# Kernel tuning notes

Measured on AMD Instinct MI355X. Metric: run time of the kernel, lower is better.

## Reference

```python
import jax, jax.numpy as jnp
import numpy as np

N_NODES = 50000
N_EDGES = 1600000
IN_DIM = 128
OUT_DIM = 128
NUM_HEADS = 4
HEAD_DIM = OUT_DIM // NUM_HEADS


def setup_inputs() -> dict:
    key = jax.random.key(0)
    ks = jax.random.split(key, 10)
    s_in = 1.0 / np.sqrt(IN_DIM)
    s_out = 1.0 / np.sqrt(OUT_DIM)
    return {
        "x": jax.random.normal(ks[0], (N_NODES, IN_DIM), dtype=jnp.float32),
        "edge_index": jax.random.randint(ks[1], (2, N_EDGES), 0, N_NODES, dtype=jnp.int64),
        "Wq": jax.random.uniform(ks[2], (OUT_DIM, IN_DIM), jnp.float32, -s_in, s_in),
        "bq": jax.random.uniform(ks[3], (OUT_DIM,), jnp.float32, -s_in, s_in),
        "Wk": jax.random.uniform(ks[4], (OUT_DIM, IN_DIM), jnp.float32, -s_in, s_in),
        "bk": jax.random.uniform(ks[5], (OUT_DIM,), jnp.float32, -s_in, s_in),
        "Wv": jax.random.uniform(ks[6], (OUT_DIM, IN_DIM), jnp.float32, -s_in, s_in),
        "bv": jax.random.uniform(ks[7], (OUT_DIM,), jnp.float32, -s_in, s_in),
        "Wo": jax.random.uniform(ks[8], (OUT_DIM, OUT_DIM), jnp.float32, -s_out, s_out),
        "bo": jax.random.uniform(ks[9], (OUT_DIM,), jnp.float32, -s_out, s_out),
    }


def reference(x, edge_index, Wq, bq, Wk, bk, Wv, bv, Wo, bo):
    n = x.shape[0]
    # node-level projections -> [N, H, Hd]
    Q = (x @ Wq.T + bq).reshape(n, NUM_HEADS, HEAD_DIM)
    K = (x @ Wk.T + bk).reshape(n, NUM_HEADS, HEAD_DIM)
    V = (x @ Wv.T + bv).reshape(n, NUM_HEADS, HEAD_DIM)
    src, dst = edge_index[0], edge_index[1]
    # edge scores: [E, H]
    scores = (Q[dst] * K[src]).sum(-1) / np.sqrt(HEAD_DIM).astype(np.float32)
    # global-max shifted exp (faithful to original, which uses a single global max)
    scores_exp = jnp.exp(scores - scores.max())
    # per-dst normalization: [N, H]
    scores_sum = jax.ops.segment_sum(scores_exp, dst, num_segments=n)
    attention = scores_exp / (scores_sum[dst] + 1e-8)  # dropout in eval mode = identity
    # weighted aggregate of V[src] into dst: [N, H, Hd]
    messages = V[src] * attention[:, :, None]
    out = jax.ops.segment_sum(messages, dst, num_segments=n)
    out = out.reshape(n, OUT_DIM) @ Wo.T + bo
    return jax.nn.relu(out)
```

## Files before the change

### kernel.cpp

```cpp
#include <hip/hip_runtime.h>

#define N_NODES 50000
#define N_EDGES 1600000
#define DIM 128
#define M_PAD 50048
#define SCAN_NB ((N_NODES + 255) / 256)

#define OFF_WCATB  0UL
#define OFF_BCAT   98304UL
#define OFF_XB     99840UL
#define OFF_C      12912128UL
#define OFF_SRC    64112128UL
#define OFF_RANK   67312128UL
#define OFF_RS     70512128UL
#define OFF_CNT    70712136UL
#define OFF_BSUM   70912136UL
#define OFF_AGG    70913168UL

typedef __attribute__((ext_vector_type(8))) short short8;
typedef __attribute__((ext_vector_type(4))) float floatx4;

__device__ __forceinline__ unsigned bf16r(float f) {
    unsigned u = __float_as_uint(f);
    return (u + 0x7fffu + ((u >> 16) & 1u)) >> 16;
}
__device__ __forceinline__ unsigned pack2(float a, float b) {
    return bf16r(a) | (bf16r(b) << 16);
}
__device__ __forceinline__ float blo(unsigned v) { return __uint_as_float(v << 16); }
__device__ __forceinline__ float bhi(unsigned v) { return __uint_as_float(v & 0xffff0000u); }

#define CVT_NB 6250
#define ZERO_NB SCAN_NB
#define PREPW_NB 192
__global__ __launch_bounds__(256) void k_prep(const float* __restrict__ x,
                                              unsigned short* __restrict__ xb,
                                              int* __restrict__ counts,
                                              const float* __restrict__ Wq, const float* __restrict__ bq,
                                              const float* __restrict__ Wk, const float* __restrict__ bk,
                                              const float* __restrict__ Wv, const float* __restrict__ bv,
                                              unsigned short* __restrict__ Wcatb,
                                              float* __restrict__ bcat) {
    int bx = blockIdx.x, t = threadIdx.x;
    if (bx < CVT_NB) {
        int i = bx * 256 + t;
        if (i < N_NODES * DIM / 4) {
            float4 f = ((const float4*)x)[i];
            ushort4 o;
            o.x = (unsigned short)bf16r(f.x); o.y = (unsigned short)bf16r(f.y);
            o.z = (unsigned short)bf16r(f.z); o.w = (unsigned short)bf16r(f.w);
            ((ushort4*)xb)[i] = o;
        }
    } else if (bx < CVT_NB + ZERO_NB) {
        int i = (bx - CVT_NB) * 256 + t;
        if (i < N_NODES) counts[i] = 0;
    } else {
        int i = (bx - CVT_NB - ZERO_NB) * 256 + t;
        if (i < 3 * DIM * DIM) {
            int ro = i >> 7, col = i & 127;
            const float* W = (ro < 128) ? Wq : (ro < 256) ? Wk : Wv;
            Wcatb[i] = (unsigned short)bf16r(W[(ro & 127) * DIM + col]);
        }
        if (i < 3 * DIM) {
            const float* b = (i < 128) ? bq : (i < 256) ? bk : bv;
            bcat[i] = b[i & 127];
        }
    }
}

#define GQ_MB (M_PAD / 64)
#define GQ_BLOCKS (GQ_MB * 6)
#define HIST_NB 6250
#define GQH_GRID (1564 * 7)
__global__ __launch_bounds__(256) void k_gemmqkv_hist(const unsigned short* __restrict__ xb,
                                                      const unsigned short* __restrict__ Wb,
                                                      const float* __restrict__ bias,
                                                      unsigned* __restrict__ Cu, int M,
                                                      const int* __restrict__ dstA,
                                                      int* __restrict__ counts,
                                                      unsigned short* __restrict__ rank16) {
    __shared__ __align__(16) unsigned short As[64][136];
    __shared__ __align__(16) unsigned short Bs[64][136];
    const int grp = blockIdx.x / 7, r = blockIdx.x % 7;
    if (r >= 3) {
        int h = grp * 4 + (r - 3);
        if (h < HIST_NB) {
            int e = h * 256 + threadIdx.x;
            if (e < N_EDGES) rank16[e] = (unsigned short)atomicAdd(&counts[dstA[e]], 1);
        }
        return;
    }
    const int g = grp * 3 + r;
    const int m0 = (g % GQ_MB) * 64, n0 = (g / GQ_MB) * 64;
    const int t = threadIdx.x;
    {
        int row = t >> 2, ch = t & 3;
        const uint4* xrow = (const uint4*)(xb + (long)(m0 + row) * 128);
        const uint4* wrow = (const uint4*)(Wb + (long)(n0 + row) * 128);
#pragma unroll
        for (int j = 0; j < 4; ++j) {
            *(uint4*)&As[row][(ch + 4 * j) * 8] = xrow[ch + 4 * j];
            *(uint4*)&Bs[row][(ch + 4 * j) * 8] = wrow[ch + 4 * j];
        }
    }
    __syncthreads();
    const int w = t >> 6, lane = t & 63;
    const int quad = lane >> 4, c = lane & 15;
    floatx4 acc[4] = {{0.f,0.f,0.f,0.f},{0.f,0.f,0.f,0.f},{0.f,0.f,0.f,0.f},{0.f,0.f,0.f,0.f}};
#pragma unroll
    for (int ks = 0; ks < 4; ++ks) {
        short8 a = *(const short8*)&As[w * 16 + c][ks * 32 + quad * 8];
#pragma unroll
        for (int nt = 0; nt < 4; ++nt) {
            short8 b = *(const short8*)&Bs[nt * 16 + c][ks * 32 + quad * 8];
            acc[nt] = __builtin_amdgcn_mfma_f32_16x16x32_bf16(a, b, acc[nt], 0, 0, 0);
        }
    }
#pragma unroll
    for (int nt = 0; nt < 4; ++nt) {
        int gn = n0 + nt * 16 + c;
        float bv = bias[gn];
        int slice = gn >> 7;
        int cs = gn & 127;
#pragma unroll
        for (int i = 0; i < 4; ++i) {
            int gm = m0 + w * 16 + quad * 4 + i;
            float o = acc[nt][i] + bv;
            float f1 = __shfl_xor(o, 1);
            float f2 = __shfl_xor(o, 2);
            float f3 = __shfl_xor(o, 3);
            if (gm < M) {
                unsigned* crow = Cu + (long)gm * 256;
                if (slice == 0) {
                    ((float*)crow)[cs] = o;
                } else if (slice == 1) {
                    if ((c & 3) == 0) {
                        int pk = __builtin_amdgcn_cvt_pk_fp8_f32(o, f1, 0, false);
                        pk = __builtin_amdgcn_cvt_pk_fp8_f32(f2, f3, pk, true);
                        crow[128 + (cs >> 2)] = (unsigned)pk;
                    }
                } else {
                    if ((c & 1) == 0) crow[160 + (cs >> 1)] = pack2(o, f1);
                }
            }
        }
    }
}

__global__ __launch_bounds__(256) void k_scanA(const int* __restrict__ counts,
                                               int* __restrict__ bsum) {
    __shared__ int red[256];
    int t = threadIdx.x, i = blockIdx.x * 256 + t;
    red[t] = (i < N_NODES) ? counts[i] : 0;
    __syncthreads();
    for (int off = 128; off > 0; off >>= 1) {
        if (t < off) red[t] += red[t + off];
        __syncthreads();
    }
    if (t == 0) bsum[blockIdx.x] = red[0];
}
__global__ __launch_bounds__(256) void k_scanB(int* __restrict__ bsum, int nb) {
    __shared__ int s[256];
    int t = threadIdx.x;
    int v = (t < nb) ? bsum[t] : 0;
    s[t] = v;
    __syncthreads();
    for (int off = 1; off < 256; off <<= 1) {
        int u = (t >= off) ? s[t - off] : 0;
        __syncthreads();
        s[t] += u;
        __syncthreads();
    }
    if (t < nb) bsum[t] = s[t] - v;
}
__global__ __launch_bounds__(256) void k_scanC(const int* __restrict__ counts,
                                               const int* __restrict__ bsum,
                                               int* __restrict__ row_start) {
    __shared__ int s[256];
    int t = threadIdx.x, i = blockIdx.x * 256 + t;
    int v = (i < N_NODES) ? counts[i] : 0;
    s[t] = v;
    __syncthreads();
    for (int off = 1; off < 256; off <<= 1) {
        int u = (t >= off) ? s[t - off] : 0;
        __syncthreads();
        s[t] += u;
        __syncthreads();
    }
    int excl = bsum[blockIdx.x] + s[t] - v;
    if (i < N_NODES) {
        row_start[i] = excl;
        if (i == N_NODES - 1) row_start[N_NODES] = excl + v;
    }
}

__global__ void k_fill(const int* __restrict__ srcA, const int* __restrict__ dstA,
                       const int* __restrict__ row_start,
                       const unsigned short* __restrict__ rank16,
                       unsigned short* __restrict__ csr_src) {
    int e = blockIdx.x * blockDim.x + threadIdx.x;
    if (e < N_EDGES) {
        int d = dstA[e];
        csr_src[row_start[d] + rank16[e]] = (unsigned short)srcA[e];
    }
}

__global__ __launch_bounds__(256) void k_attn(const unsigned* __restrict__ Cu,
                                              const int* __restrict__ row_start,
                                              const unsigned short* __restrict__ csr_src,
                                              float* __restrict__ agg) {
    int d = blockIdx.x * 4 + (threadIdx.x >> 6);
    int lane = threadIdx.x & 63;
    if (d >= N_NODES) return;
    const int half = lane >> 5, sl = lane & 31;
    const float scale = 0.17677669529663687f;
    float4 q4 = *(const float4*)((const float*)(Cu + (long)d * 256) + 4 * sl);
    q4.x *= scale; q4.y *= scale; q4.z *= scale; q4.w *= scale;
    int s0 = row_start[d], s1 = row_start[d + 1];
    float lsum = 0.f, a0 = 0.f, a1 = 0.f, a2 = 0.f, a3 = 0.f;
    int pos = s0;
    for (; pos + 4 <= s1; pos += 4) {
        int sa = csr_src[pos + half];
        int sb = csr_src[pos + 2 + half];
        const unsigned* ra = Cu + (long)sa * 256;
        const unsigned* rb = Cu + (long)sb * 256;
        unsigned ka = ra[128 + sl];
        unsigned kb = rb[128 + sl];
        uint2 va = *(const uint2*)(ra + 160 + 2 * sl);
        uint2 vb = *(const uint2*)(rb + 160 + 2 * sl);
        float pa = q4.x * __builtin_amdgcn_cvt_f32_fp8(ka, 0)
                 + q4.y * __builtin_amdgcn_cvt_f32_fp8(ka, 1)
                 + q4.z * __builtin_amdgcn_cvt_f32_fp8(ka, 2)
                 + q4.w * __builtin_amdgcn_cvt_f32_fp8(ka, 3);
        float pb = q4.x * __builtin_amdgcn_cvt_f32_fp8(kb, 0)
                 + q4.y * __builtin_amdgcn_cvt_f32_fp8(kb, 1)
                 + q4.z * __builtin_amdgcn_cvt_f32_fp8(kb, 2)
                 + q4.w * __builtin_amdgcn_cvt_f32_fp8(kb, 3);
        pa += __shfl_xor(pa, 1); pa += __shfl_xor(pa, 2); pa += __shfl_xor(pa, 4);
        pb += __shfl_xor(pb, 1); pb += __shfl_xor(pb, 2); pb += __shfl_xor(pb, 4);
        float wa = __expf(pa), wb = __expf(pb);
        lsum += wa + wb;
        a0 += wa * blo(va.x) + wb * blo(vb.x);
        a1 += wa * bhi(va.x) + wb * bhi(vb.x);
        a2 += wa * blo(va.y) + wb * blo(vb.y);
        a3 += wa * bhi(va.y) + wb * bhi(vb.y);
    }
    for (; pos < s1; pos += 2) {
        int e = pos + half;
        bool ok = e < s1;
        int sa = csr_src[ok ? e : (s1 - 1)];
        const unsigned* ra = Cu + (long)sa * 256;
        unsigned ka = ra[128 + sl];
        uint2 va = *(const uint2*)(ra + 160 + 2 * sl);
        float pa = q4.x * __builtin_amdgcn_cvt_f32_fp8(ka, 0)
                 + q4.y * __builtin_amdgcn_cvt_f32_fp8(ka, 1)
                 + q4.z * __builtin_amdgcn_cvt_f32_fp8(ka, 2)
                 + q4.w * __builtin_amdgcn_cvt_f32_fp8(ka, 3);
        pa += __shfl_xor(pa, 1); pa += __shfl_xor(pa, 2); pa += __shfl_xor(pa, 4);
        float wa = ok ? __expf(pa) : 0.f;
        lsum += wa;
        a0 += wa * blo(va.x);
        a1 += wa * bhi(va.x);
        a2 += wa * blo(va.y);
        a3 += wa * bhi(va.y);
    }
    lsum += __shfl_xor(lsum, 32);
    a0 += __shfl_xor(a0, 32);
    a1 += __shfl_xor(a1, 32);
    a2 += __shfl_xor(a2, 32);
    a3 += __shfl_xor(a3, 32);
    if (lane < 32) {
        float inv = 1.f / (lsum + 1e-8f);
        float4 o;
        o.x = a0 * inv; o.y = a1 * inv; o.z = a2 * inv; o.w = a3 * inv;
        *(float4*)&agg[(long)d * 128 + 4 * sl] = o;
    }
}

__global__ __launch_bounds__(256) void k_gemm(const float* __restrict__ A,
                                              const float* __restrict__ B,
                                              const float* __restrict__ bias,
                                              float* __restrict__ Cp, int M) {
    __shared__ float As[32][64];
    __shared__ float Bs[32][64];
    const int m0 = blockIdx.x * 64, n0 = blockIdx.y * 64;
    const int t = threadIdx.x;
    const int tm = (t & 15) * 4, tn = (t >> 4) * 4;
    float acc[4][4] = {};
    for (int k0 = 0; k0 < 128; k0 += 32) {
#pragma unroll
        for (int i = 0; i < 2; ++i) {
            int idx = t + i * 256;
            int row = idx >> 3;
            int c4 = (idx & 7) * 4;
            float4 fa = make_float4(0.f, 0.f, 0.f, 0.f);
            if (m0 + row < M) fa = *(const float4*)&A[(long)(m0 + row) * 128 + k0 + c4];
            As[c4 + 0][row] = fa.x; As[c4 + 1][row] = fa.y;
            As[c4 + 2][row] = fa.z; As[c4 + 3][row] = fa.w;
            float4 fb = *(const float4*)&B[(long)(n0 + row) * 128 + k0 + c4];
            Bs[c4 + 0][row] = fb.x; Bs[c4 + 1][row] = fb.y;
            Bs[c4 + 2][row] = fb.z; Bs[c4 + 3][row] = fb.w;
        }
        __syncthreads();
#pragma unroll
        for (int k = 0; k < 32; ++k) {
            float4 a = *(const float4*)&As[k][tm];
            float4 b = *(const float4*)&Bs[k][tn];
            acc[0][0] += a.x * b.x; acc[0][1] += a.x * b.y; acc[0][2] += a.x * b.z; acc[0][3] += a.x * b.w;
            acc[1][0] += a.y * b.x; acc[1][1] += a.y * b.y; acc[1][2] += a.y * b.z; acc[1][3] += a.y * b.w;
            acc[2][0] += a.z * b.x; acc[2][1] += a.z * b.y; acc[2][2] += a.z * b.z; acc[2][3] += a.z * b.w;
            acc[3][0] += a.w * b.x; acc[3][1] += a.w * b.y; acc[3][2] += a.w * b.z; acc[3][3] += a.w * b.w;
        }
        __syncthreads();
    }
    float4 bv4 = *(const float4*)&bias[n0 + tn];
#pragma unroll
    for (int i = 0; i < 4; ++i) {
        int m = m0 + tm + i;
        if (m >= M) continue;
        float4 o;
        o.x = fmaxf(acc[i][0] + bv4.x, 0.f); o.y = fmaxf(acc[i][1] + bv4.y, 0.f);
        o.z = fmaxf(acc[i][2] + bv4.z, 0.f); o.w = fmaxf(acc[i][3] + bv4.w, 0.f);
        *(float4*)&Cp[(long)m * 128 + n0 + tn] = o;
    }
}

extern "C" void kernel_launch(void* const* d_in, const int* in_sizes, int n_in,
                              void* d_out, int out_size, void* d_ws, size_t ws_size,
                              hipStream_t stream) {
    const float* x  = (const float*)d_in[0];
    const int* edge = (const int*)d_in[1];
    const float* Wq = (const float*)d_in[2];
    const float* bq = (const float*)d_in[3];
    const float* Wk = (const float*)d_in[4];
    const float* bk = (const float*)d_in[5];
    const float* Wv = (const float*)d_in[6];
    const float* bv = (const float*)d_in[7];
    const float* Wo = (const float*)d_in[8];
    const float* bo = (const float*)d_in[9];
    float* out = (float*)d_out;

    char* ws = (char*)d_ws;
    unsigned short* Wcatb = (unsigned short*)(ws + OFF_WCATB);
    float* bcat      = (float*)(ws + OFF_BCAT);
    unsigned short* xb = (unsigned short*)(ws + OFF_XB);
    unsigned* Cu     = (unsigned*)(ws + OFF_C);
    unsigned short* csr_src = (unsigned short*)(ws + OFF_SRC);
    unsigned short* rank16  = (unsigned short*)(ws + OFF_RANK);
    int*   row_start = (int*)(ws + OFF_RS);
    int*   counts    = (int*)(ws + OFF_CNT);
    int*   bsum      = (int*)(ws + OFF_BSUM);
    float* agg       = (float*)(ws + OFF_AGG);

    const int* srcA = edge;
    const int* dstA = edge + N_EDGES;

    k_prep<<<CVT_NB + ZERO_NB + PREPW_NB, 256, 0, stream>>>(
        x, xb, counts, Wq, bq, Wk, bk, Wv, bv, Wcatb, bcat);

    k_gemmqkv_hist<<<GQH_GRID, 256, 0, stream>>>(
        xb, Wcatb, bcat, Cu, N_NODES, dstA, counts, rank16);

    k_scanA<<<SCAN_NB, 256, 0, stream>>>(counts, bsum);
    k_scanB<<<1, 256, 0, stream>>>(bsum, SCAN_NB);
    k_scanC<<<SCAN_NB, 256, 0, stream>>>(counts, bsum, row_start);
    k_fill<<<(N_EDGES + 255) / 256, 256, 0, stream>>>(srcA, dstA, row_start, rank16, csr_src);

    k_attn<<<(N_NODES + 3) / 4, 256, 0, stream>>>(Cu, row_start, csr_src, agg);

    k_gemm<<<dim3((N_NODES + 63) / 64, 2), 256, 0, stream>>>(agg, Wo, bo, out, N_NODES);
}
```

Baseline: 319.0 us.

## Move histogram into prep kernel and fuse CSR fill with QKV GEMM

Moves the dst-degree histogram atomics into the input-conversion kernel, interleaved block-by-block with the x-to-bf16 conversion. The CSR fill step now runs inside the QKV GEMM launch as extra blocks, so the scatter overlaps the MFMA work instead of being a separate launch. The counter zeroing becomes a hipMemsetAsync. This removes one kernel launch and rebalances memory-bound and compute-bound work across launches, but adds a memset call and an extra stage boundary before the GEMM.

```diff
diff --git a/kernel.cpp b/kernel.cpp
--- a/kernel.cpp
+++ b/kernel.cpp
@@ -30,32 +30,37 @@
 __device__ __forceinline__ float blo(unsigned v) { return __uint_as_float(v << 16); }
 __device__ __forceinline__ float bhi(unsigned v) { return __uint_as_float(v & 0xffff0000u); }
 
-#define CVT_NB 6250
-#define ZERO_NB SCAN_NB
+#define PH_PAIRS 6250
 #define PREPW_NB 192
-__global__ __launch_bounds__(256) void k_prep(const float* __restrict__ x,
-                                              unsigned short* __restrict__ xb,
-                                              int* __restrict__ counts,
-                                              const float* __restrict__ Wq, const float* __restrict__ bq,
-                                              const float* __restrict__ Wk, const float* __restrict__ bk,
-                                              const float* __restrict__ Wv, const float* __restrict__ bv,
-                                              unsigned short* __restrict__ Wcatb,
-                                              float* __restrict__ bcat) {
+#define PH_GRID (2 * PH_PAIRS + PREPW_NB)
+__global__ __launch_bounds__(256) void k_prep_hist(const float* __restrict__ x,
+                                                   unsigned short* __restrict__ xb,
+                                                   const float* __restrict__ Wq, const float* __restrict__ bq,
+                                                   const float* __restrict__ Wk, const float* __restrict__ bk,
+                                                   const float* __restrict__ Wv, const float* __restrict__ bv,
+                                                   unsigned short* __restrict__ Wcatb,
+                                                   float* __restrict__ bcat,
+                                                   const int* __restrict__ dstA,
+                                                   int* __restrict__ counts,
+                                                   unsigned short* __restrict__ rank16) {
     int bx = blockIdx.x, t = threadIdx.x;
-    if (bx < CVT_NB) {
-        int i = bx * 256 + t;
-        if (i < N_NODES * DIM / 4) {
-            float4 f = ((const float4*)x)[i];
-            ushort4 o;
-            o.x = (unsigned short)bf16r(f.x); o.y = (unsigned short)bf16r(f.y);
-            o.z = (unsigned short)bf16r(f.z); o.w = (unsigned short)bf16r(f.w);
-            ((ushort4*)xb)[i] = o;
-        }
-    } else if (bx < CVT_NB + ZERO_NB) {
-        int i = (bx - CVT_NB) * 256 + t;
-        if (i < N_NODES) counts[i] = 0;
+    if (bx < 2 * PH_PAIRS) {
+        int pair = bx >> 1;
+        if (bx & 1) {
+            int i = pair * 256 + t;
+            if (i < N_NODES * DIM / 4) {
+                float4 f = ((const float4*)x)[i];
+                ushort4 o;
+                o.x = (unsigned short)bf16r(f.x); o.y = (unsigned short)bf16r(f.y);
+                o.z = (unsigned short)bf16r(f.z); o.w = (unsigned short)bf16r(f.w);
+                ((ushort4*)xb)[i] = o;
+            }
+        } else {
+            int e = pair * 256 + t;
+            if (e < N_EDGES) rank16[e] = (unsigned short)atomicAdd(&counts[dstA[e]], 1);
+        }
     } else {
-        int i = (bx - CVT_NB - ZERO_NB) * 256 + t;
+        int i = (bx - 2 * PH_PAIRS) * 256 + t;
         if (i < 3 * DIM * DIM) {
             int ro = i >> 7, col = i & 127;
             const float* W = (ro < 128) ? Wq : (ro < 256) ? Wk : Wv;
@@ -68,29 +73,83 @@
     }
 }
 
+__global__ __launch_bounds__(256) void k_scanA(const int* __restrict__ counts,
+                                               int* __restrict__ bsum) {
+    __shared__ int red[256];
+    int t = threadIdx.x, i = blockIdx.x * 256 + t;
+    red[t] = (i < N_NODES) ? counts[i] : 0;
+    __syncthreads();
+    for (int off = 128; off > 0; off >>= 1) {
+        if (t < off) red[t] += red[t + off];
+        __syncthreads();
+    }
+    if (t == 0) bsum[blockIdx.x] = red[0];
+}
+__global__ __launch_bounds__(256) void k_scanB(int* __restrict__ bsum, int nb) {
+    __shared__ int s[256];
+    int t = threadIdx.x;
+    int v = (t < nb) ? bsum[t] : 0;
+    s[t] = v;
+    __syncthreads();
+    for (int off = 1; off < 256; off <<= 1) {
+        int u = (t >= off) ? s[t - off] : 0;
+        __syncthreads();
+        s[t] += u;
+        __syncthreads();
+    }
+    if (t < nb) bsum[t] = s[t] - v;
+}
+__global__ __launch_bounds__(256) void k_scanC(const int* __restrict__ counts,
+                                               const int* __restrict__ bsum,
+                                               int* __restrict__ row_start) {
+    __shared__ int s[256];
+    int t = threadIdx.x, i = blockIdx.x * 256 + t;
+    int v = (i < N_NODES) ? counts[i] : 0;
+    s[t] = v;
+    __syncthreads();
+    for (int off = 1; off < 256; off <<= 1) {
+        int u = (t >= off) ? s[t - off] : 0;
+        __syncthreads();
+        s[t] += u;
+        __syncthreads();
+    }
+    int excl = bsum[blockIdx.x] + s[t] - v;
+    if (i < N_NODES) {
+        row_start[i] = excl;
+        if (i == N_NODES - 1) row_start[N_NODES] = excl + v;
+    }
+}
+
 #define GQ_MB (M_PAD / 64)
 #define GQ_BLOCKS (GQ_MB * 6)
-#define HIST_NB 6250
-#define GQH_GRID (1564 * 7)
-__global__ __launch_bounds__(256) void k_gemmqkv_hist(const unsigned short* __restrict__ xb,
+#define FILL_NB 6250
+#define GF_GRPS 1564
+#define GF_GRID (GF_GRPS * 7)
+__global__ __launch_bounds__(256) void k_gemmqkv_fill(const unsigned short* __restrict__ xb,
                                                       const unsigned short* __restrict__ Wb,
                                                       const float* __restrict__ bias,
                                                       unsigned* __restrict__ Cu, int M,
+                                                      const int* __restrict__ srcA,
                                                       const int* __restrict__ dstA,
-                                                      int* __restrict__ counts,
-                                                      unsigned short* __restrict__ rank16) {
+                                                      const int* __restrict__ row_start,
+                                                      const unsigned short* __restrict__ rank16,
+                                                      unsigned short* __restrict__ csr_src) {
     __shared__ __align__(16) unsigned short As[64][136];
     __shared__ __align__(16) unsigned short Bs[64][136];
     const int grp = blockIdx.x / 7, r = blockIdx.x % 7;
-    if (r >= 3) {
-        int h = grp * 4 + (r - 3);
-        if (h < HIST_NB) {
-            int e = h * 256 + threadIdx.x;
-            if (e < N_EDGES) rank16[e] = (unsigned short)atomicAdd(&counts[dstA[e]], 1);
+    if (r < 4) {
+        int fb = grp * 4 + r;
+        if (fb < FILL_NB) {
+            int e = fb * 256 + threadIdx.x;
+            if (e < N_EDGES) {
+                int d = dstA[e];
+                csr_src[row_start[d] + rank16[e]] = (unsigned short)srcA[e];
+            }
         }
         return;
     }
-    const int g = grp * 3 + r;
+    const int g = grp * 3 + (r - 4);
+    if (g >= GQ_BLOCKS) return;
     const int m0 = (g % GQ_MB) * 64, n0 = (g / GQ_MB) * 64;
     const int t = threadIdx.x;
     {
@@ -144,64 +203,6 @@
                 }
             }
         }
-    }
-}
-
-__global__ __launch_bounds__(256) void k_scanA(const int* __restrict__ counts,
-                                               int* __restrict__ bsum) {
-    __shared__ int red[256];
-    int t = threadIdx.x, i = blockIdx.x * 256 + t;
-    red[t] = (i < N_NODES) ? counts[i] : 0;
-    __syncthreads();
-    for (int off = 128; off > 0; off >>= 1) {
-        if (t < off) red[t] += red[t + off];
-        __syncthreads();
-    }
-    if (t == 0) bsum[blockIdx.x] = red[0];
-}
-__global__ __launch_bounds__(256) void k_scanB(int* __restrict__ bsum, int nb) {
-    __shared__ int s[256];
-    int t = threadIdx.x;
-    int v = (t < nb) ? bsum[t] : 0;
-    s[t] = v;
-    __syncthreads();
-    for (int off = 1; off < 256; off <<= 1) {
-        int u = (t >= off) ? s[t - off] : 0;
-        __syncthreads();
-        s[t] += u;
-        __syncthreads();
-    }
-    if (t < nb) bsum[t] = s[t] - v;
-}
-__global__ __launch_bounds__(256) void k_scanC(const int* __restrict__ counts,
-                                               const int* __restrict__ bsum,
-                                               int* __restrict__ row_start) {
-    __shared__ int s[256];
-    int t = threadIdx.x, i = blockIdx.x * 256 + t;
-    int v = (i < N_NODES) ? counts[i] : 0;
-    s[t] = v;
-    __syncthreads();
-    for (int off = 1; off < 256; off <<= 1) {
-        int u = (t >= off) ? s[t - off] : 0;
-        __syncthreads();
-        s[t] += u;
-        __syncthreads();
-    }
-    int excl = bsum[blockIdx.x] + s[t] - v;
-    if (i < N_NODES) {
-        row_start[i] = excl;
-        if (i == N_NODES - 1) row_start[N_NODES] = excl + v;
-    }
-}
-
-__global__ void k_fill(const int* __restrict__ srcA, const int* __restrict__ dstA,
-                       const int* __restrict__ row_start,
-                       const unsigned short* __restrict__ rank16,
-                       unsigned short* __restrict__ csr_src) {
-    int e = blockIdx.x * blockDim.x + threadIdx.x;
-    if (e < N_EDGES) {
-        int d = dstA[e];
-        csr_src[row_start[d] + rank16[e]] = (unsigned short)srcA[e];
     }
 }
 
@@ -355,16 +356,17 @@
     const int* srcA = edge;
     const int* dstA = edge + N_EDGES;
 
-    k_prep<<<CVT_NB + ZERO_NB + PREPW_NB, 256, 0, stream>>>(
-        x, xb, counts, Wq, bq, Wk, bk, Wv, bv, Wcatb, bcat);
-
-    k_gemmqkv_hist<<<GQH_GRID, 256, 0, stream>>>(
-        xb, Wcatb, bcat, Cu, N_NODES, dstA, counts, rank16);
+    hipMemsetAsync(counts, 0, N_NODES * 4, stream);
+
+    k_prep_hist<<<PH_GRID, 256, 0, stream>>>(
+        x, xb, Wq, bq, Wk, bk, Wv, bv, Wcatb, bcat, dstA, counts, rank16);
 
     k_scanA<<<SCAN_NB, 256, 0, stream>>>(counts, bsum);
     k_scanB<<<1, 256, 0, stream>>>(bsum, SCAN_NB);
     k_scanC<<<SCAN_NB, 256, 0, stream>>>(counts, bsum, row_start);
-    k_fill<<<(N_EDGES + 255) / 256, 256, 0, stream>>>(srcA, dstA, row_start, rank16, csr_src);
+
+    k_gemmqkv_fill<<<GF_GRID, 256, 0, stream>>>(
+        xb, Wcatb, bcat, Cu, N_NODES, srcA, dstA, row_start, rank16, csr_src);
 
     k_attn<<<(N_NODES + 3) / 4, 256, 0, stream>>>(Cu, row_start, csr_src, agg);
 
```

Measured after the change: 329.2 us. 1.03x slower.
